# Optimization experiments

Hardware: AMD Instinct MI355X
Metric: run time of the kernel (lower is better)

## Reference

```python
import jax, jax.numpy as jnp
import numpy as np

T = 16384      # total packed tokens
C = 1024       # d_model
H = 16         # n_head
HD = C // H    # head dim = 64
N_SEG = 32     # number of equal varlen segments
SEG = T // N_SEG


def setup_inputs() -> dict:
    key = jax.random.key(0)
    k1, k2, k3 = jax.random.split(key, 3)
    x = jax.random.normal(k1, (T, C), dtype=jnp.float32)
    w_attn = jax.random.normal(k2, (C, 3 * C), dtype=jnp.float32) * (1.0 / np.sqrt(C))
    w_proj = jax.random.normal(k3, (C, C), dtype=jnp.float32) * (1.0 / np.sqrt(C))
    # boundary indices for torch.tensor_split -> 32 equal segments of SEG tokens
    split_sections = (jnp.arange(1, N_SEG) * SEG).astype(jnp.int64)
    return {"x": x, "w_attn": w_attn, "w_proj": w_proj, "split_sections": split_sections}


def reference(x, w_attn, w_proj, split_sections):
    # x: [T, C] packed tokens; split_sections: 31 boundaries -> 32 equal segments
    n_seg = int(np.asarray(split_sections).shape[0]) + 1
    seg = x.shape[0] // n_seg
    qkv = x @ w_attn                                   # [T, 3C]
    q, k, v = jnp.split(qkv, 3, axis=-1)               # each [T, C]

    def heads(t):
        # [T, C] -> [H, n_seg, seg, HD]  (block-diagonal segment layout)
        return t.reshape(x.shape[0], H, HD).transpose(1, 0, 2).reshape(H, n_seg, seg, HD)

    q, k, v = heads(q), heads(k), heads(v)
    scale = 1.0 / np.sqrt(HD)
    att = jnp.einsum('hnqd,hnkd->hnqk', q, k) * scale  # [H, n_seg, seg, seg]
    att = jax.nn.softmax(att, axis=-1)
    y = jnp.einsum('hnqk,hnkd->hnqd', att, v)          # [H, n_seg, seg, HD]
    y = y.reshape(H, x.shape[0], HD).transpose(1, 0, 2).reshape(x.shape[0], C)
    return y @ w_proj                                  # [T, C]
```

## Files before the change

### kernel.cpp

```cpp
#include <hip/hip_runtime.h>
#include <hip/hip_bf16.h>
#include <stdint.h>

typedef __attribute__((ext_vector_type(8))) short short8;
typedef __attribute__((ext_vector_type(4))) short short4_t;
typedef __attribute__((ext_vector_type(4))) float float4_t;
typedef __attribute__((ext_vector_type(4))) float f4;

#define GLOAD_LDS16(gp, lp)                                                              \
  __builtin_amdgcn_global_load_lds((const __attribute__((address_space(1))) unsigned int*)(gp), \
                                   (__attribute__((address_space(3))) unsigned int*)(lp), \
                                   16, 0, 0)

__device__ __forceinline__ float4_t mfma_bf16(short8 a, short8 b, float4_t c) {
  return __builtin_amdgcn_mfma_f32_16x16x32_bf16(a, b, c, 0, 0, 0);
}

__device__ __forceinline__ short f2bf(float f) {
  union { float f; unsigned int u; } v; v.f = f;
  unsigned int r = v.u + 0x7fff + ((v.u >> 16) & 1);
  return (short)(r >> 16);
}

__device__ __forceinline__ float red_sum16(float v) {
  v += __shfl_xor(v, 1);
  v += __shfl_xor(v, 2);
  v += __shfl_xor(v, 4);
  v += __shfl_xor(v, 8);
  return v;
}

__device__ __forceinline__ long swz_col(long colbase64, int chunk, int sub, int row) {
  return colbase64 + ((chunk ^ (row & 7)) << 3) + sub;
}

__global__ __launch_bounds__(256) void conv_swz(const float* __restrict__ in,
                                                short* __restrict__ out, long nchunks) {
  for (long ch = (long)blockIdx.x * blockDim.x + threadIdx.x; ch < nchunks;
       ch += (long)gridDim.x * blockDim.x) {
    long r  = ch >> 7;
    int cir = (int)(ch & 127);
    int pc  = (cir & ~7) | ((cir & 7) ^ ((int)r & 7));
    const float* src = in + ch * 8;
    f4 f0 = *(const f4*)(src);
    f4 f1 = *(const f4*)(src + 4);
    short8 o;
#pragma unroll
    for (int j = 0; j < 4; ++j) o[j] = f2bf(f0[j]);
#pragma unroll
    for (int j = 0; j < 4; ++j) o[4 + j] = f2bf(f1[j]);
    *(short8*)&out[r * 1024 + pc * 8] = o;
  }
}

template <int SWZ64>
__global__ __launch_bounds__(256) void transpose_conv(const float* __restrict__ in,
                                                      short* __restrict__ out,
                                                      int R, int C) {
  __shared__ short tile[32][33];
  int c0 = blockIdx.x * 32;
  int r0 = blockIdx.y * 32;
  int tx = threadIdx.x;
  int ty = threadIdx.y;
#pragma unroll
  for (int i = 0; i < 4; ++i)
    tile[ty + i * 8][tx] = f2bf(in[(long)(r0 + ty + i * 8) * C + c0 + tx]);
  __syncthreads();
#pragma unroll
  for (int i = 0; i < 4; ++i) {
    int n   = c0 + ty + i * 8;
    int col = r0 + tx;
    long cc;
    if constexpr (SWZ64) {
      cc = swz_col((long)(col & ~63), (col >> 3) & 7, col & 7, n);
    } else {
      cc = (long)r0 + ((((tx >> 3) ^ ((n >> 1) & 3))) << 3) + (tx & 7);
    }
    out[(long)n * R + cc] = tile[tx][ty + i * 8];
  }
}

__global__ __launch_bounds__(256, 2) void gemm_bt(const short* __restrict__ A, long lda,
                                                  const short* __restrict__ Bt,
                                                  short* __restrict__ Cq,
                                                  short* __restrict__ vT,
                                                  int M, int N, int K, int mbase) {
  __shared__ __align__(16) short As[128 * 64];
  __shared__ __align__(16) short Bs[128 * 64];

  const int tid  = threadIdx.x;
  const int wave = tid >> 6;
  const int lane = tid & 63;
  const int rA   = lane & 15;
  const int q4   = lane >> 4;
  const long m0  = ((long)blockIdx.y + mbase) * 128;
  const long n0  = (long)blockIdx.x * 128;
  const int wm   = (wave & 1) * 64;
  const int wn   = (wave >> 1) * 64;

  float4_t acc[4][4];
#pragma unroll
  for (int i = 0; i < 4; ++i)
#pragma unroll
    for (int j = 0; j < 4; ++j) acc[i][j] = (float4_t){0.f, 0.f, 0.f, 0.f};

  for (int k0 = 0; k0 < K; k0 += 64) {
#pragma unroll
    for (int i = 0; i < 4; ++i) {
      int slot = i * 256 + tid;
      int r    = slot >> 3;
      int c    = slot & 7;
      const short* ga = A  + (m0 + r) * lda      + k0 + c * 8;
      const short* gb = Bt + (n0 + r) * (long)K  + k0 + c * 8;
      GLOAD_LDS16(ga, &As[(i * 256 + wave * 64) * 8]);
      GLOAD_LDS16(gb, &Bs[(i * 256 + wave * 64) * 8]);
    }
    __syncthreads();
#pragma unroll
    for (int kk = 0; kk < 2; ++kk) {
      int cp = (kk * 4 + q4) ^ (rA & 7);
      short8 af[4], bfr[4];
#pragma unroll
      for (int mi = 0; mi < 4; ++mi) {
        int r  = wm + mi * 16 + rA;
        af[mi] = *(const short8*)&As[(r * 8 + cp) * 8];
      }
#pragma unroll
      for (int ni = 0; ni < 4; ++ni) {
        int r  = wn + ni * 16 + rA;
        bfr[ni] = *(const short8*)&Bs[(r * 8 + cp) * 8];
      }
#pragma unroll
      for (int mi = 0; mi < 4; ++mi)
#pragma unroll
        for (int ni = 0; ni < 4; ++ni)
          acc[mi][ni] = mfma_bf16(af[mi], bfr[ni], acc[mi][ni]);
    }
    __syncthreads();
  }

  if (n0 >= 2048) {
#pragma unroll
    for (int mi = 0; mi < 4; ++mi) {
      int tbase = (int)m0 + wm + mi * 16 + q4 * 4;
      int ct    = (tbase >> 3) & 7;
#pragma unroll
      for (int ni = 0; ni < 4; ++ni) {
        int c = (int)n0 + wn + ni * 16 + rA;
        int d = c - 2048;
        long dst = (long)d * 16384 + (long)(tbase & ~63) +
                   (((ct ^ (d & 7))) << 3) + (tbase & 7);
        short4_t o;
#pragma unroll
        for (int reg = 0; reg < 4; ++reg) o[reg] = f2bf(acc[mi][ni][reg]);
        *(short4_t*)&vT[dst] = o;
      }
    }
  } else {
#pragma unroll
    for (int mi = 0; mi < 4; ++mi)
#pragma unroll
      for (int ni = 0; ni < 4; ++ni)
#pragma unroll
        for (int reg = 0; reg < 4; ++reg) {
          long t = m0 + wm + mi * 16 + q4 * 4 + reg;
          int  c = (int)n0 + wn + ni * 16 + rA;
          long cc = swz_col((long)(c & ~63), (c >> 3) & 7, c & 7, (int)t);
          Cq[t * 3072 + cc] = f2bf(acc[mi][ni][reg]);
        }
  }
}

__global__ __launch_bounds__(512, 2) void gemm256(const short* __restrict__ A, long lda,
                                                  const short* __restrict__ Bt, long ldb,
                                                  float* __restrict__ Co,
                                                  int M, int N, int K) {
  __shared__ __align__(16) short As[4][256 * 32];
  __shared__ __align__(16) short Bs[4][256 * 32];

  const int tid  = threadIdx.x;
  const int wave = tid >> 6;
  const int lane = tid & 63;
  const int rA   = lane & 15;
  const int q4   = lane >> 4;
  const int wm   = (wave >> 2) * 128;
  const int wn   = (wave & 3) * 64;

  const int nbx = N >> 8;
  const int nwg = nbx * (M >> 8);
  const int bid = (int)blockIdx.y * nbx + (int)blockIdx.x;
  const int cpx = nwg >> 3;
  const int swz = (bid & 7) * cpx + (bid >> 3);
  const long m0 = (long)(swz / nbx) * 256;
  const long n0 = (long)(swz % nbx) * 256;

  const short* Ag = A  + (m0 + (tid >> 2)) * lda + (tid & 3) * 8;
  const short* Bg = Bt + (n0 + (tid >> 2)) * ldb + (tid & 3) * 8;

#define STAGE_A(u)                                                          \
  {                                                                         \
    const int slot_ = (u) & 3;                                              \
    GLOAD_LDS16(Ag + (u) * 32,             &As[slot_][wave * 512]);         \
    GLOAD_LDS16(Ag + 128 * lda + (u) * 32, &As[slot_][4096 + wave * 512]);  \
  }
#define STAGE_B(u)                                                          \
  {                                                                         \
    const int slot_ = (u) & 3;                                              \
    GLOAD_LDS16(Bg + (u) * 32,             &Bs[slot_][wave * 512]);         \
    GLOAD_LDS16(Bg + 128 * ldb + (u) * 32, &Bs[slot_][4096 + wave * 512]);  \
  }

  float4_t acc[8][4];
#pragma unroll
  for (int i = 0; i < 8; ++i)
#pragma unroll
    for (int j = 0; j < 4; ++j) acc[i][j] = (float4_t){0.f, 0.f, 0.f, 0.f};

  const int nt = K >> 5;
  const int cswz = q4 ^ ((rA >> 1) & 3);

  STAGE_A(0); STAGE_B(0);
  STAGE_A(1); STAGE_B(1);
  STAGE_A(2); STAGE_B(2);
  asm volatile("s_waitcnt vmcnt(8)" ::: "memory");
  __builtin_amdgcn_s_barrier();

  short8 afl[4], afh[4], bf0[4], bf1[4];
#pragma unroll
  for (int mi = 0; mi < 4; ++mi)
    afl[mi] = *(const short8*)&As[0][((wm + mi * 16 + rA) * 4 + cswz) * 8];
#pragma unroll
  for (int ni = 0; ni < 4; ++ni)
    bf0[ni] = *(const short8*)&Bs[0][((wn + ni * 16 + rA) * 4 + cswz) * 8];

  auto tile_step = [&](int u, short8 (&bc)[4], short8 (&bn)[4]) {
    const int slot = u & 3;
#pragma unroll
    for (int mi = 0; mi < 4; ++mi)
      afh[mi] = *(const short8*)&As[slot][((wm + 64 + mi * 16 + rA) * 4 + cswz) * 8];
    if (u + 3 < nt) STAGE_A(u + 3);
    asm volatile("s_waitcnt lgkmcnt(4)" ::: "memory");
    __builtin_amdgcn_s_setprio(1);
#pragma unroll
    for (int mi = 0; mi < 4; ++mi)
#pragma unroll
      for (int ni = 0; ni < 4; ++ni)
        acc[mi][ni] = mfma_bf16(afl[mi], bc[ni], acc[mi][ni]);
    __builtin_amdgcn_s_setprio(0);
    if (u + 3 < nt)      asm volatile("s_waitcnt vmcnt(6)" ::: "memory");
    else if (u + 2 < nt) asm volatile("s_waitcnt vmcnt(4)" ::: "memory");
    else                 asm volatile("s_waitcnt vmcnt(0)" ::: "memory");
    __builtin_amdgcn_s_barrier();
    if (u + 1 < nt) {
      const int ns = (u + 1) & 3;
#pragma unroll
      for (int mi = 0; mi < 4; ++mi)
        afl[mi] = *(const short8*)&As[ns][((wm + mi * 16 + rA) * 4 + cswz) * 8];
#pragma unroll
      for (int ni = 0; ni < 4; ++ni)
        bn[ni] = *(const short8*)&Bs[ns][((wn + ni * 16 + rA) * 4 + cswz) * 8];
    }
    if (u + 3 < nt) STAGE_B(u + 3);
    if (u + 1 < nt) asm volatile("s_waitcnt lgkmcnt(8)" ::: "memory");
    else            asm volatile("s_waitcnt lgkmcnt(0)" ::: "memory");
    __builtin_amdgcn_s_setprio(1);
#pragma unroll
    for (int mi = 0; mi < 4; ++mi)
#pragma unroll
      for (int ni = 0; ni < 4; ++ni)
        acc[mi + 4][ni] = mfma_bf16(afh[mi], bc[ni], acc[mi + 4][ni]);
    __builtin_amdgcn_s_setprio(0);
    __builtin_amdgcn_s_barrier();
  };

  for (int u = 0; u < nt; u += 2) {
    tile_step(u,     bf0, bf1);
    tile_step(u + 1, bf1, bf0);
  }
#undef STAGE_A
#undef STAGE_B

#pragma unroll
  for (int mi = 0; mi < 8; ++mi)
#pragma unroll
    for (int ni = 0; ni < 4; ++ni)
#pragma unroll
      for (int reg = 0; reg < 4; ++reg) {
        long row = m0 + wm + mi * 16 + q4 * 4 + reg;
        long col = n0 + wn + ni * 16 + rA;
        Co[row * (long)N + col] = acc[mi][ni][reg];
      }
}

__global__ __launch_bounds__(512, 2) void attn_kernel(short* __restrict__ qkv,
                                                      const short* __restrict__ vT) {
  __shared__ __align__(16) short Qs[512 * 64];
  __shared__ __align__(16) short Ks[2][64 * 64];
  __shared__ __align__(16) short Vt[64 * 64];
  __shared__ __align__(16) short Ps[512 * 64];

  const int tid  = threadIdx.x;
  const int wave = tid >> 6;
  const int lane = tid & 63;
  const int rA   = lane & 15;
  const int q4   = lane >> 4;
  const int seg  = blockIdx.x;
  const int h    = blockIdx.y;

  const long tq0  = (long)seg * 512;
  const long tk0  = (long)seg * 512;
  const long hoff = (long)h * 64;

#pragma unroll
  for (int i = 0; i < 8; ++i) {
    int slot = i * 512 + tid;
    int r    = slot >> 3;
    int c    = slot & 7;
    GLOAD_LDS16(qkv + (tq0 + r) * 3072 + hoff + c * 8, &Qs[(i * 512 + wave * 64) * 8]);
  }
  {
    int r = tid >> 3;
    int c = tid & 7;
    GLOAD_LDS16(qkv + (tk0 + r) * 3072 + 1024 + hoff + c * 8, &Ks[0][(wave * 64) * 8]);
  }

  float4_t acc_o[4][4];
  float l_st[4][4];
#pragma unroll
  for (int mi = 0; mi < 4; ++mi)
#pragma unroll
    for (int di = 0; di < 4; ++di) acc_o[mi][di] = (float4_t){0.f, 0.f, 0.f, 0.f};
#pragma unroll
  for (int mi = 0; mi < 4; ++mi)
#pragma unroll
    for (int reg = 0; reg < 4; ++reg) l_st[mi][reg] = 0.f;

  for (int kt = 0; kt < 8; ++kt) {
    const int p = kt & 1;
    __syncthreads();

    {
      int r = tid >> 3;
      int c = tid & 7;
      GLOAD_LDS16(vT + (hoff + r) * 16384 + tk0 + kt * 64 + c * 8, &Vt[(wave * 64) * 8]);
      if (kt < 7)
        GLOAD_LDS16(qkv + (tk0 + (kt + 1) * 64 + r) * 3072 + 1024 + hoff + c * 8,
                    &Ks[1 - p][(wave * 64) * 8]);
    }

    float4_t s_acc[4][4];
#pragma unroll
    for (int mi = 0; mi < 4; ++mi)
#pragma unroll
      for (int ni = 0; ni < 4; ++ni) s_acc[mi][ni] = (float4_t){0.f, 0.f, 0.f, 0.f};
#pragma unroll
    for (int kk = 0; kk < 2; ++kk) {
      int cp = (kk * 4 + q4) ^ (rA & 7);
      short8 af[4], bfr[4];
#pragma unroll
      for (int mi = 0; mi < 4; ++mi) {
        int r  = wave * 64 + mi * 16 + rA;
        af[mi] = *(const short8*)&Qs[(r * 8 + cp) * 8];
      }
#pragma unroll
      for (int ni = 0; ni < 4; ++ni) {
        int r  = ni * 16 + rA;
        bfr[ni] = *(const short8*)&Ks[p][(r * 8 + cp) * 8];
      }
      __builtin_amdgcn_s_setprio(1);
#pragma unroll
      for (int mi = 0; mi < 4; ++mi)
#pragma unroll
        for (int ni = 0; ni < 4; ++ni)
          s_acc[mi][ni] = mfma_bf16(af[mi], bfr[ni], s_acc[mi][ni]);
      __builtin_amdgcn_s_setprio(0);
    }

#pragma unroll
    for (int mi = 0; mi < 4; ++mi)
#pragma unroll
      for (int reg = 0; reg < 4; ++reg) {
        float rs = 0.f;
#pragma unroll
        for (int ni = 0; ni < 4; ++ni) {
          float pv = __expf(s_acc[mi][ni][reg] * 0.125f);
          s_acc[mi][ni][reg] = pv;
          rs += pv;
        }
        l_st[mi][reg] += rs;
      }

#pragma unroll
    for (int mi = 0; mi < 4; ++mi)
#pragma unroll
      for (int ni = 0; ni < 4; ++ni)
#pragma unroll
        for (int reg = 0; reg < 4; ++reg) {
          int row = wave * 64 + mi * 16 + q4 * 4 + reg;
          int col = ni * 16 + rA;
          Ps[row * 64 + (((col >> 3) ^ (row & 7)) << 3) + (col & 7)] =
              f2bf(s_acc[mi][ni][reg]);
        }

    __syncthreads();

#pragma unroll
    for (int kk = 0; kk < 2; ++kk) {
      int cp = (kk * 4 + q4) ^ (rA & 7);
      short8 af[4], bfr[4];
#pragma unroll
      for (int mi = 0; mi < 4; ++mi) {
        int row = wave * 64 + mi * 16 + rA;
        af[mi] = *(const short8*)&Ps[row * 64 + cp * 8];
      }
#pragma unroll
      for (int di = 0; di < 4; ++di)
        bfr[di] = *(const short8*)&Vt[((di * 16 + rA) * 8 + cp) * 8];
      __builtin_amdgcn_s_setprio(1);
#pragma unroll
      for (int mi = 0; mi < 4; ++mi)
#pragma unroll
        for (int di = 0; di < 4; ++di)
          acc_o[mi][di] = mfma_bf16(af[mi], bfr[di], acc_o[mi][di]);
      __builtin_amdgcn_s_setprio(0);
    }
  }

#pragma unroll
  for (int mi = 0; mi < 4; ++mi)
#pragma unroll
    for (int reg = 0; reg < 4; ++reg) {
      float l  = red_sum16(l_st[mi][reg]);
      float rl = 1.0f / l;
      long t = tq0 + wave * 64 + mi * 16 + q4 * 4 + reg;
#pragma unroll
      for (int di = 0; di < 4; ++di) {
        int c  = di * 16 + rA;
        long cc = hoff + (c & 32) +
                  (((((c >> 3) & 3) ^ (((int)t >> 1) & 3))) << 3) + (c & 7);
        qkv[t * 3072 + cc] = f2bf(acc_o[mi][di][reg] * rl);
      }
    }
}

extern "C" void kernel_launch(void* const* d_in, const int* in_sizes, int n_in,
                              void* d_out, int out_size, void* d_ws, size_t ws_size,
                              hipStream_t stream) {
  const float* x      = (const float*)d_in[0];
  const float* w_attn = (const float*)d_in[1];
  const float* w_proj = (const float*)d_in[2];
  float* out = (float*)d_out;

  short* wT_a = (short*)d_ws;
  short* wT_p = wT_a + (size_t)3072 * 1024;
  short* qkv  = wT_p + (size_t)1024 * 1024;

  short* xb = (short*)d_out;
  short* vT = xb + (size_t)16384 * 1024;

  conv_swz<<<2048, 256, 0, stream>>>(x, xb, (long)16384 * 1024 / 8);
  transpose_conv<1><<<dim3(3072 / 32, 1024 / 32), dim3(32, 8), 0, stream>>>(w_attn, wT_a, 1024, 3072);
  transpose_conv<0><<<dim3(1024 / 32, 1024 / 32), dim3(32, 8), 0, stream>>>(w_proj, wT_p, 1024, 1024);

  for (int c = 0; c < 4; ++c)
    gemm_bt<<<dim3(3072 / 128, 32), 256, 0, stream>>>(xb, 1024, wT_a, qkv, vT,
                                                      16384, 3072, 1024, c * 32);

  attn_kernel<<<dim3(32, 16), 512, 0, stream>>>(qkv, vT);

  gemm256<<<dim3(1024 / 256, 16384 / 256), 512, 0, stream>>>(qkv, 3072, wT_p, 1024, out,
                                                             16384, 1024, 1024);
}
```

Baseline: 381.2 us.

## Split attention blocks by query half, keep Q in registers, double-buffer V

The attention kernel now runs 256-thread blocks that each handle half of a segment's queries, launching 1024 blocks where there were 512. Q fragments are held in registers so the Q shared buffer can be reused for P, and V is double-buffered alongside K. The mid-iteration block barrier becomes a per-wave lgkmcnt wait, which is safe because each wave only reads its own P rows. The QKV GEMM is issued as two launches of 64 row-tiles instead of four of 32. This cuts per-block LDS and barrier cost and gives more blocks to fill the machine, at the price of higher register pressure and K/V being loaded twice per segment.

```diff
diff --git a/kernel.cpp b/kernel.cpp
--- a/kernel.cpp
+++ b/kernel.cpp
@@ -292,37 +292,56 @@
       }
 }
 
-__global__ __launch_bounds__(512, 2) void attn_kernel(short* __restrict__ qkv,
+__global__ __launch_bounds__(256, 2) void attn_kernel(short* __restrict__ qkv,
                                                       const short* __restrict__ vT) {
-  __shared__ __align__(16) short Qs[512 * 64];
+  __shared__ __align__(16) short QP[256 * 64];
   __shared__ __align__(16) short Ks[2][64 * 64];
-  __shared__ __align__(16) short Vt[64 * 64];
-  __shared__ __align__(16) short Ps[512 * 64];
+  __shared__ __align__(16) short Vt[2][64 * 64];
 
   const int tid  = threadIdx.x;
   const int wave = tid >> 6;
   const int lane = tid & 63;
   const int rA   = lane & 15;
   const int q4   = lane >> 4;
-  const int seg  = blockIdx.x;
-  const int h    = blockIdx.y;
-
-  const long tq0  = (long)seg * 512;
+  const int qh   = blockIdx.x;
+  const int seg  = blockIdx.y;
+  const int h    = blockIdx.z;
+
+  const long tq0  = (long)seg * 512 + qh * 256;
   const long tk0  = (long)seg * 512;
   const long hoff = (long)h * 64;
 
 #pragma unroll
   for (int i = 0; i < 8; ++i) {
-    int slot = i * 512 + tid;
+    int slot = i * 256 + tid;
     int r    = slot >> 3;
     int c    = slot & 7;
-    GLOAD_LDS16(qkv + (tq0 + r) * 3072 + hoff + c * 8, &Qs[(i * 512 + wave * 64) * 8]);
-  }
-  {
-    int r = tid >> 3;
-    int c = tid & 7;
-    GLOAD_LDS16(qkv + (tk0 + r) * 3072 + 1024 + hoff + c * 8, &Ks[0][(wave * 64) * 8]);
-  }
+    GLOAD_LDS16(qkv + (tq0 + r) * 3072 + hoff + c * 8, &QP[(i * 256 + wave * 64) * 8]);
+  }
+#pragma unroll
+  for (int i = 0; i < 2; ++i) {
+    int slot = i * 256 + tid;
+    int r    = slot >> 3;
+    int c    = slot & 7;
+    GLOAD_LDS16(qkv + (tk0 + r) * 3072 + 1024 + hoff + c * 8,
+                &Ks[0][(i * 256 + wave * 64) * 8]);
+    GLOAD_LDS16(vT + (hoff + r) * 16384 + tk0 + c * 8,
+                &Vt[0][(i * 256 + wave * 64) * 8]);
+  }
+  __syncthreads();
+
+  short8 qreg[2][4];
+#pragma unroll
+  for (int kk = 0; kk < 2; ++kk) {
+    int cp = (kk * 4 + q4) ^ (rA & 7);
+#pragma unroll
+    for (int mi = 0; mi < 4; ++mi) {
+      int r = wave * 64 + mi * 16 + rA;
+      qreg[kk][mi] = *(const short8*)&QP[(r * 8 + cp) * 8];
+    }
+  }
+  asm volatile("s_waitcnt lgkmcnt(0)" ::: "memory");
+  __builtin_amdgcn_sched_barrier(0);
 
   float4_t acc_o[4][4];
   float l_st[4][4];
@@ -337,15 +356,18 @@
 
   for (int kt = 0; kt < 8; ++kt) {
     const int p = kt & 1;
-    __syncthreads();
-
-    {
-      int r = tid >> 3;
-      int c = tid & 7;
-      GLOAD_LDS16(vT + (hoff + r) * 16384 + tk0 + kt * 64 + c * 8, &Vt[(wave * 64) * 8]);
-      if (kt < 7)
-        GLOAD_LDS16(qkv + (tk0 + (kt + 1) * 64 + r) * 3072 + 1024 + hoff + c * 8,
-                    &Ks[1 - p][(wave * 64) * 8]);
+    if (kt < 7) {
+      const long tkn = tk0 + (kt + 1) * 64;
+#pragma unroll
+      for (int i = 0; i < 2; ++i) {
+        int slot = i * 256 + tid;
+        int r    = slot >> 3;
+        int c    = slot & 7;
+        GLOAD_LDS16(qkv + (tkn + r) * 3072 + 1024 + hoff + c * 8,
+                    &Ks[1 - p][(i * 256 + wave * 64) * 8]);
+        GLOAD_LDS16(vT + (hoff + r) * 16384 + tkn + c * 8,
+                    &Vt[1 - p][(i * 256 + wave * 64) * 8]);
+      }
     }
 
     float4_t s_acc[4][4];
@@ -356,23 +378,16 @@
 #pragma unroll
     for (int kk = 0; kk < 2; ++kk) {
       int cp = (kk * 4 + q4) ^ (rA & 7);
-      short8 af[4], bfr[4];
-#pragma unroll
-      for (int mi = 0; mi < 4; ++mi) {
-        int r  = wave * 64 + mi * 16 + rA;
-        af[mi] = *(const short8*)&Qs[(r * 8 + cp) * 8];
-      }
-#pragma unroll
-      for (int ni = 0; ni < 4; ++ni) {
-        int r  = ni * 16 + rA;
-        bfr[ni] = *(const short8*)&Ks[p][(r * 8 + cp) * 8];
-      }
+      short8 bfr[4];
+#pragma unroll
+      for (int ni = 0; ni < 4; ++ni)
+        bfr[ni] = *(const short8*)&Ks[p][((ni * 16 + rA) * 8 + cp) * 8];
       __builtin_amdgcn_s_setprio(1);
 #pragma unroll
       for (int mi = 0; mi < 4; ++mi)
 #pragma unroll
         for (int ni = 0; ni < 4; ++ni)
-          s_acc[mi][ni] = mfma_bf16(af[mi], bfr[ni], s_acc[mi][ni]);
+          s_acc[mi][ni] = mfma_bf16(qreg[kk][mi], bfr[ni], s_acc[mi][ni]);
       __builtin_amdgcn_s_setprio(0);
     }
 
@@ -398,11 +413,11 @@
         for (int reg = 0; reg < 4; ++reg) {
           int row = wave * 64 + mi * 16 + q4 * 4 + reg;
           int col = ni * 16 + rA;
-          Ps[row * 64 + (((col >> 3) ^ (row & 7)) << 3) + (col & 7)] =
+          QP[row * 64 + (((col >> 3) ^ (row & 7)) << 3) + (col & 7)] =
               f2bf(s_acc[mi][ni][reg]);
         }
-
-    __syncthreads();
+    asm volatile("s_waitcnt lgkmcnt(0)" ::: "memory");
+    __builtin_amdgcn_sched_barrier(0);
 
 #pragma unroll
     for (int kk = 0; kk < 2; ++kk) {
@@ -411,11 +426,11 @@
 #pragma unroll
       for (int mi = 0; mi < 4; ++mi) {
         int row = wave * 64 + mi * 16 + rA;
-        af[mi] = *(const short8*)&Ps[row * 64 + cp * 8];
+        af[mi] = *(const short8*)&QP[(row * 8 + cp) * 8];
       }
 #pragma unroll
       for (int di = 0; di < 4; ++di)
-        bfr[di] = *(const short8*)&Vt[((di * 16 + rA) * 8 + cp) * 8];
+        bfr[di] = *(const short8*)&Vt[p][((di * 16 + rA) * 8 + cp) * 8];
       __builtin_amdgcn_s_setprio(1);
 #pragma unroll
       for (int mi = 0; mi < 4; ++mi)
@@ -424,6 +439,9 @@
           acc_o[mi][di] = mfma_bf16(af[mi], bfr[di], acc_o[mi][di]);
       __builtin_amdgcn_s_setprio(0);
     }
+
+    asm volatile("s_waitcnt vmcnt(0)" ::: "memory");
+    __builtin_amdgcn_s_barrier();
   }
 
 #pragma unroll
@@ -462,11 +480,11 @@
   transpose_conv<1><<<dim3(3072 / 32, 1024 / 32), dim3(32, 8), 0, stream>>>(w_attn, wT_a, 1024, 3072);
   transpose_conv<0><<<dim3(1024 / 32, 1024 / 32), dim3(32, 8), 0, stream>>>(w_proj, wT_p, 1024, 1024);
 
-  for (int c = 0; c < 4; ++c)
-    gemm_bt<<<dim3(3072 / 128, 32), 256, 0, stream>>>(xb, 1024, wT_a, qkv, vT,
-                                                      16384, 3072, 1024, c * 32);
-
-  attn_kernel<<<dim3(32, 16), 512, 0, stream>>>(qkv, vT);
+  for (int c = 0; c < 2; ++c)
+    gemm_bt<<<dim3(3072 / 128, 64), 256, 0, stream>>>(xb, 1024, wT_a, qkv, vT,
+                                                      16384, 3072, 1024, c * 64);
+
+  attn_kernel<<<dim3(2, 32, 16), 256, 0, stream>>>(qkv, vT);
 
   gemm256<<<dim3(1024 / 256, 16384 / 256), 512, 0, stream>>>(qkv, 3072, wT_p, 1024, out,
                                                              16384, 1024, 1024);
```

Result: slower. 537.9 us (+41.1%).
